# Optimization experiments

Measured on AMD Instinct MI355X. Metric: run time of the kernel, lower is better.

Reference implementation:

```python
import jax, jax.numpy as jnp
import numpy as np

B, S, H, K = 64, 512, 768, 21  # batch, seq_len, bert hidden, num_labels


def setup_inputs() -> dict:
    key = jax.random.key(0)
    ks = jax.random.split(key, 8)
    hidden = jax.random.normal(ks[0], (B, S, H), jnp.float32)  # post-BERT states
    W = jax.random.normal(ks[1], (H, K), jnp.float32) * 0.02    # classifier weight
    b = jnp.zeros((K,), jnp.float32)                            # classifier bias
    start_transitions = jax.random.uniform(ks[2], (K,), jnp.float32, -0.1, 0.1)
    transitions = jax.random.uniform(ks[3], (K, K), jnp.float32, -0.1, 0.1)
    end_transitions = jax.random.uniform(ks[4], (K,), jnp.float32, -0.1, 0.1)
    labels = jax.random.randint(ks[5], (B, S), 0, K)
    # torchcrf requires mask[:, 0] == 1; use variable-length prefix masks
    lengths = jax.random.randint(ks[6], (B,), S // 2, S + 1)
    attention_mask = jnp.arange(S)[None, :] < lengths[:, None]  # [B,S] bool
    return dict(hidden=hidden, W=W, b=b,
                start_transitions=start_transitions,
                transitions=transitions,
                end_transitions=end_transitions,
                labels=labels, attention_mask=attention_mask)


def _crf_nll(logits, labels, mask, start_t, trans, end_t):
    """torchcrf CRF forward (reduction='sum' log-likelihood), negated."""
    fmask = mask.astype(logits.dtype)  # [B,S]
    # ---- numerator: score of the gold path ----
    emit = jnp.take_along_axis(logits, labels[..., None], axis=2)[..., 0]  # [B,S]
    tr = trans[labels[:, :-1], labels[:, 1:]]                              # [B,S-1]
    num = start_t[labels[:, 0]] + emit[:, 0] \
        + jnp.sum((emit[:, 1:] + tr) * fmask[:, 1:], axis=1)
    lengths = mask.sum(axis=1)
    last_tags = jnp.take_along_axis(labels, (lengths - 1)[:, None], axis=1)[:, 0]
    num = num + end_t[last_tags]
    # ---- denominator: forward algorithm (logsumexp recurrence) ----
    alpha0 = start_t[None, :] + logits[:, 0]           # [B,K]
    ems = jnp.swapaxes(logits[:, 1:], 0, 1)            # [S-1,B,K]
    ms = jnp.swapaxes(mask[:, 1:], 0, 1)               # [S-1,B]

    def step(alpha, xs):
        em, m = xs
        nxt = jax.scipy.special.logsumexp(
            alpha[:, :, None] + trans[None, :, :] + em[:, None, :], axis=1)
        return jnp.where(m[:, None], nxt, alpha), None

    alpha, _ = jax.lax.scan(step, alpha0, (ems, ms))
    logZ = jax.scipy.special.logsumexp(alpha + end_t[None, :], axis=1)  # [B]
    return jnp.sum(logZ - num)  # negative log-likelihood (sum over batch)


def reference(hidden, W, b, start_transitions, transitions, end_transitions,
              labels, attention_mask):
    # dropout is identity in eval; the GRU in __init__ is unused in forward
    logits = hidden @ W + b  # [B,S,K]
    nll = _crf_nll(logits, labels, attention_mask,
                   start_transitions, transitions, end_transitions)
    # module returns (logits, -1 * log_likelihood) = (logits, nll)
    return (logits, nll)
```

## Files before the change

kernel.cpp:

```cpp
#include <hip/hip_runtime.h>

#define BSZ 64
#define SEQ 512
#define HID 768
#define NK  21

typedef short bf16x8 __attribute__((ext_vector_type(8)));
typedef float f32x4  __attribute__((ext_vector_type(4)));

__device__ __forceinline__ unsigned f2bf1(float x) {
    unsigned u = __float_as_uint(x);
    return (u + 0x7fffu + ((u >> 16) & 1u)) >> 16;
}
__device__ __forceinline__ unsigned f2bf_pk(float lo, float hi) {
    return f2bf1(lo) | (f2bf1(hi) << 16);
}

__global__ __launch_bounds__(256) void wconv_kernel(
    const float* __restrict__ W, unsigned short* __restrict__ WT)
{
    const int idx = blockIdx.x * 256 + threadIdx.x;
    const int n = idx / HID;
    const int k = idx - n * HID;
    unsigned short v = 0;
    if (n < NK) v = (unsigned short)f2bf1(W[(size_t)k * NK + n]);
    WT[idx] = v;
}

__global__ __launch_bounds__(256) void gemm_bias_kernel(
    const float* __restrict__ hidden, const unsigned short* __restrict__ WT,
    const float* __restrict__ bias, float* __restrict__ out)
{
    const int tid  = threadIdx.x;
    const int lane = tid & 63;
    const int wv   = tid >> 6;
    const int n    = lane & 15;
    const int quad = lane >> 4;

    const int arow = blockIdx.x * 64 + wv * 16 + n;
    const float* ap = hidden + (size_t)arow * HID + quad * 8;
    const bf16x8* bp0 = (const bf16x8*)(WT + (size_t)n * HID + quad * 8);
    const bf16x8* bp1 = (const bf16x8*)(WT + (size_t)(16 + n) * HID + quad * 8);

    f32x4 acc0 = {0.f, 0.f, 0.f, 0.f};
    f32x4 acc1 = {0.f, 0.f, 0.f, 0.f};

    float4 c0a = *(const float4*)(ap + 0);
    float4 c0b = *(const float4*)(ap + 4);

    #pragma unroll
    for (int c = 0; c < HID / 32; ++c) {
        float4 c1a, c1b;
        if (c + 1 < HID / 32) {
            c1a = *(const float4*)(ap + (c + 1) * 32);
            c1b = *(const float4*)(ap + (c + 1) * 32 + 4);
        }
        union { bf16x8 v; unsigned u[4]; } af;
        af.u[0] = f2bf_pk(c0a.x, c0a.y);
        af.u[1] = f2bf_pk(c0a.z, c0a.w);
        af.u[2] = f2bf_pk(c0b.x, c0b.y);
        af.u[3] = f2bf_pk(c0b.z, c0b.w);

        const bf16x8 b0 = bp0[c * 4];
        const bf16x8 b1 = bp1[c * 4];

        acc0 = __builtin_amdgcn_mfma_f32_16x16x32_bf16(af.v, b0, acc0, 0, 0, 0);
        acc1 = __builtin_amdgcn_mfma_f32_16x16x32_bf16(af.v, b1, acc1, 0, 0, 0);
        c0a = c1a; c0b = c1b;
    }

    const float b0v = bias[n];
    const float b1v = (n < NK - 16) ? bias[16 + n] : 0.f;
    const int rbase = blockIdx.x * 64 + wv * 16 + quad * 4;
    #pragma unroll
    for (int r = 0; r < 4; ++r) {
        float* op = out + (size_t)(rbase + r) * NK;
        op[n] = acc0[r] + b0v;
        if (n < NK - 16) op[16 + n] = acc1[r] + b1v;
    }
}

__global__ __launch_bounds__(128) void crf_kernel(
    const float* __restrict__ logits,
    const float* __restrict__ start_t,
    const float* __restrict__ trans,
    const float* __restrict__ end_t,
    const int* __restrict__ labels,
    const int* __restrict__ mask,
    float* __restrict__ per_batch)
{
    __shared__ __align__(16) float Xl[SEQ * NK];
    __shared__ float C[SEQ];
    __shared__ float comb[24];

    const int b    = blockIdx.x;
    const int tid  = threadIdx.x;
    const int lane = tid & 63;
    const int wid  = tid >> 6;

    {
        const float4* g4 = (const float4*)(logits + (size_t)b * SEQ * NK);
        float4* l4 = (float4*)Xl;
        for (int idx = tid; idx < SEQ * NK / 4; idx += 128) l4[idx] = g4[idx];
    }

    const int* lab = labels + b * SEQ;
    const int* msk = mask   + b * SEQ;

    int cnt = 0;
    for (int t = lane; t < SEQ; t += 64) cnt += (msk[t] != 0);
    #pragma unroll
    for (int off = 32; off > 0; off >>= 1) cnt += __shfl_xor(cnt, off, 64);
    const int L = cnt;
    const int m = L >> 1;

    __syncthreads();

    {
        float numacc = 0.f;
        for (int t = tid; t < L; t += 128) {
            if (t == 0) numacc += start_t[lab[0]] + Xl[lab[0]];
            else        numacc += Xl[t * NK + lab[t]] + trans[lab[t - 1] * NK + lab[t]];
        }
        if (tid == 0) numacc += end_t[lab[L - 1]];
        #pragma unroll
        for (int off = 32; off > 0; off >>= 1) numacc += __shfl_xor(numacc, off, 64);
        if (lane == 0) comb[22 + wid] = numacc;
    }

    for (int t = tid; t < SEQ; t += 128) C[t] = Xl[t * NK];
    __syncthreads();

    for (int idx = tid; idx < SEQ * NK; idx += 128) {
        const int t = idx / NK;
        Xl[idx] = __expf(Xl[idx] - C[t]);
    }
    __syncthreads();

    const int jj = (lane < NK) ? lane : NK - 1;

#define BP(v, k) __uint_as_float(__builtin_amdgcn_ds_bpermute(4 * (k), __float_as_uint(v)))
#define MATVEC(vv, EE, outv) do {                                          \
    float s0 = BP(vv, 0) * EE[0];                                          \
    float s1 = BP(vv, 1) * EE[1];                                          \
    float s2 = BP(vv, 2) * EE[2];                                          \
    s0 = fmaf(BP(vv,  3), EE[ 3], s0); s1 = fmaf(BP(vv,  4), EE[ 4], s1);  \
    s2 = fmaf(BP(vv,  5), EE[ 5], s2); s0 = fmaf(BP(vv,  6), EE[ 6], s0);  \
    s1 = fmaf(BP(vv,  7), EE[ 7], s1); s2 = fmaf(BP(vv,  8), EE[ 8], s2);  \
    s0 = fmaf(BP(vv,  9), EE[ 9], s0); s1 = fmaf(BP(vv, 10), EE[10], s1);  \
    s2 = fmaf(BP(vv, 11), EE[11], s2); s0 = fmaf(BP(vv, 12), EE[12], s0);  \
    s1 = fmaf(BP(vv, 13), EE[13], s1); s2 = fmaf(BP(vv, 14), EE[14], s2);  \
    s0 = fmaf(BP(vv, 15), EE[15], s0); s1 = fmaf(BP(vv, 16), EE[16], s1);  \
    s2 = fmaf(BP(vv, 17), EE[17], s2); s0 = fmaf(BP(vv, 18), EE[18], s0);  \
    s1 = fmaf(BP(vv, 19), EE[19], s1); s2 = fmaf(BP(vv, 20), EE[20], s2);  \
    outv = (s0 + s1) + s2;                                                 \
} while (0)
#define RENORM() do {                                                      \
    const float mm = __uint_as_float(                                      \
        __builtin_amdgcn_readfirstlane(__float_as_uint(a)));               \
    a *= __builtin_amdgcn_rcpf(mm);                                        \
    Orenorm += __logf(mm);                                                 \
} while (0)

    float a;
    float Orenorm = 0.f;
    float csum = 0.f;

    if (wid == 0) {
        float Ecol[NK];
        #pragma unroll
        for (int k = 0; k < NK; ++k) Ecol[k] = __expf(trans[k * NK + jj]);

        a = __expf(start_t[jj]) * Xl[jj];
        for (int t = lane; t <= m; t += 64) csum += C[t];

#define FSTEP(xr) do { float nv; MATVEC(a, Ecol, nv); a = nv * (xr); } while (0)
        int t0 = 1;
        for (; t0 + 7 <= m; t0 += 8) {
            const float* xb = Xl + t0 * NK + jj;
            const float x0 = xb[0];      const float x1 = xb[NK];
            const float x2 = xb[2 * NK]; const float x3 = xb[3 * NK];
            const float x4 = xb[4 * NK]; const float x5 = xb[5 * NK];
            const float x6 = xb[6 * NK]; const float x7 = xb[7 * NK];
            FSTEP(x0); FSTEP(x1); FSTEP(x2); FSTEP(x3);
            FSTEP(x4); FSTEP(x5); FSTEP(x6); FSTEP(x7);
            RENORM();
        }
        for (; t0 <= m; ++t0) { const float x = Xl[t0 * NK + jj]; FSTEP(x); }
#undef FSTEP
    } else {
        float Erow[NK];
        #pragma unroll
        for (int k = 0; k < NK; ++k) Erow[k] = __expf(trans[jj * NK + k]);

        a = __expf(end_t[jj]);
        for (int t = m + 1 + lane; t < L; t += 64) csum += C[t];

#define BSTEP(xr) do { const float u = a * (xr); float nv; MATVEC(u, Erow, nv); a = nv; } while (0)
        int t0 = L - 1;
        for (; t0 - 7 >= m + 1; t0 -= 8) {
            const float* xb = Xl + t0 * NK + jj;
            const float x0 = xb[0];       const float x1 = xb[-NK];
            const float x2 = xb[-2 * NK]; const float x3 = xb[-3 * NK];
            const float x4 = xb[-4 * NK]; const float x5 = xb[-5 * NK];
            const float x6 = xb[-6 * NK]; const float x7 = xb[-7 * NK];
            BSTEP(x0); BSTEP(x1); BSTEP(x2); BSTEP(x3);
            BSTEP(x4); BSTEP(x5); BSTEP(x6); BSTEP(x7);
            RENORM();
        }
        for (; t0 >= m + 1; --t0) { const float x = Xl[t0 * NK + jj]; BSTEP(x); }
#undef BSTEP
    }
#undef BP
#undef MATVEC
#undef RENORM

    #pragma unroll
    for (int off = 32; off > 0; off >>= 1) csum += __shfl_xor(csum, off, 64);

    if (wid == 1) {
        if (lane < NK) comb[lane] = a;
        if (lane == 0) comb[21] = csum + Orenorm;
    }
    __syncthreads();

    if (wid == 0) {
        float val = (lane < NK) ? a * comb[lane] : 0.f;
        #pragma unroll
        for (int off = 32; off > 0; off >>= 1) val += __shfl_xor(val, off, 64);
        if (lane == 0) {
            const float OF  = csum + Orenorm;
            const float num = comb[22] + comb[23];
            per_batch[b] = OF + comb[21] + __logf(val) - num;
        }
    }
}

__global__ __launch_bounds__(64) void reduce_kernel(
    const float* __restrict__ pb, float* __restrict__ out)
{
    float v = pb[threadIdx.x];
    #pragma unroll
    for (int off = 32; off > 0; off >>= 1) v += __shfl_xor(v, off, 64);
    if (threadIdx.x == 0) out[BSZ * SEQ * NK] = v;
}

extern "C" void kernel_launch(void* const* d_in, const int* in_sizes, int n_in,
                              void* d_out, int out_size, void* d_ws, size_t ws_size,
                              hipStream_t stream)
{
    const float* hidden  = (const float*)d_in[0];
    const float* W       = (const float*)d_in[1];
    const float* bias    = (const float*)d_in[2];
    const float* start_t = (const float*)d_in[3];
    const float* trans   = (const float*)d_in[4];
    const float* end_t   = (const float*)d_in[5];
    const int*   labels  = (const int*)d_in[6];
    const int*   mask    = (const int*)d_in[7];
    float* out = (float*)d_out;

    float*          pb = (float*)d_ws;
    unsigned short* WT = (unsigned short*)((char*)d_ws + 256);

    wconv_kernel<<<(32 * HID) / 256, 256, 0, stream>>>(W, WT);
    gemm_bias_kernel<<<(BSZ * SEQ) / 64, 256, 0, stream>>>(hidden, WT, bias, out);
    crf_kernel<<<BSZ, 128, 0, stream>>>(out, start_t, trans, end_t, labels, mask, pb);
    reduce_kernel<<<1, 64, 0, stream>>>(pb, out);
}
```

Baseline: 208.3 us.

## Parallelize CRF forward recurrence via segment transfer-matrix prepass and short scan

Replaces the serial 512-step per-batch CRF recurrence with a prepass kernel that, for each of 64 segments of 8 timesteps per batch, multiplies out the 21x21 transfer matrices in parallel, normalizing and logging the scale factors. A scan kernel then chains only 32 segment matrices forward and 32 backward per batch, using readlane instead of bpermute. This aims to shorten the latency-bound sequential chain and raise occupancy. In exchange it adds a large workspace write and readback of segment matrices, more total flops, and relies on per-segment renormalization for numerical range.

```diff
diff --git a/kernel.cpp b/kernel.cpp
--- a/kernel.cpp
+++ b/kernel.cpp
@@ -4,6 +4,8 @@
 #define SEQ 512
 #define HID 768
 #define NK  21
+#define NSEG 64
+#define SEGLEN 8
 
 typedef short bf16x8 __attribute__((ext_vector_type(8)));
 typedef float f32x4  __attribute__((ext_vector_type(4)));
@@ -80,47 +82,135 @@
     }
 }
 
-__global__ __launch_bounds__(128) void crf_kernel(
+__global__ __launch_bounds__(64) void prepass_kernel(
+    const float* __restrict__ logits, const float* __restrict__ trans,
+    const int* __restrict__ mask,
+    float* __restrict__ Nrow, float* __restrict__ Ncol,
+    float* __restrict__ rlog)
+{
+    const int bs   = blockIdx.x;
+    const int b    = bs >> 6;
+    const int s    = bs & 63;
+    const int lane = threadIdx.x;
+    int g = lane / 21; if (g > 2) g = 2;
+    int i = lane - g * 21; if (i > 20) i = 20;
+    const int j0 = 7 * g;
+
+    const int* msk = mask + b * SEQ;
+    int cnt = 0;
+    #pragma unroll
+    for (int t = 0; t < SEQ / 64; ++t) cnt += (msk[lane + 64 * t] != 0);
+    #pragma unroll
+    for (int off = 32; off > 0; off >>= 1) cnt += __shfl_xor(cnt, off, 64);
+    const int L = cnt;
+
+    float E[21][7];
+    #pragma unroll
+    for (int k = 0; k < 21; ++k)
+        #pragma unroll
+        for (int jl = 0; jl < 7; ++jl)
+            E[k][jl] = __expf(trans[k * NK + j0 + jl]);
+
+    const float* lg = logits + (size_t)b * SEQ * NK;
+
+    float P[7];
+    float rl = 0.f;
+    const int t0 = s * SEGLEN + 1;
+
+    if (t0 < L) {
+        const float C = lg[t0 * NK];
+        #pragma unroll
+        for (int jl = 0; jl < 7; ++jl)
+            P[jl] = E[i][jl] * __expf(lg[t0 * NK + j0 + jl] - C);
+    } else {
+        #pragma unroll
+        for (int jl = 0; jl < 7; ++jl) P[jl] = (i == j0 + jl) ? 1.f : 0.f;
+    }
+
+#define BPF(v, idx) __uint_as_float(__builtin_amdgcn_ds_bpermute((idx) * 4, __float_as_uint(v)))
+
+    #pragma unroll
+    for (int u = 1; u < SEGLEN; ++u) {
+        const int t = t0 + u;
+        if (t < L) {
+            float row[21];
+            #pragma unroll
+            for (int k = 0; k < 21; ++k)
+                row[k] = BPF(P[k % 7], (k / 7) * 21 + i);
+
+            const float C = lg[t * NK];
+            float X[7];
+            #pragma unroll
+            for (int jl = 0; jl < 7; ++jl)
+                X[jl] = __expf(lg[t * NK + j0 + jl] - C);
+
+            #pragma unroll
+            for (int jl = 0; jl < 7; ++jl) {
+                float s0 = row[0] * E[0][jl];
+                float s1 = row[1] * E[1][jl];
+                float s2 = row[2] * E[2][jl];
+                #pragma unroll
+                for (int k = 3; k < 21; k += 3) {
+                    s0 = fmaf(row[k    ], E[k    ][jl], s0);
+                    s1 = fmaf(row[k + 1], E[k + 1][jl], s1);
+                    s2 = fmaf(row[k + 2], E[k + 2][jl], s2);
+                }
+                P[jl] = ((s0 + s1) + s2) * X[jl];
+            }
+            const float m = BPF(P[0], 0);
+            const float r = __builtin_amdgcn_rcpf(m);
+            #pragma unroll
+            for (int jl = 0; jl < 7; ++jl) P[jl] *= r;
+            rl += __logf(m);
+        }
+    }
+#undef BPF
+
+    if (lane < 63) {
+        float* nr = Nrow + (size_t)bs * 441 + i * 21 + j0;
+        #pragma unroll
+        for (int jl = 0; jl < 7; ++jl) nr[jl] = P[jl];
+        float* nc = Ncol + (size_t)bs * 441 + i;
+        #pragma unroll
+        for (int jl = 0; jl < 7; ++jl) nc[(j0 + jl) * 21] = P[jl];
+    }
+    if (lane == 0) rlog[bs] = rl;
+}
+
+__global__ __launch_bounds__(128) void scan_kernel(
     const float* __restrict__ logits,
     const float* __restrict__ start_t,
     const float* __restrict__ trans,
     const float* __restrict__ end_t,
     const int* __restrict__ labels,
     const int* __restrict__ mask,
+    const float* __restrict__ Nrow, const float* __restrict__ Ncol,
+    const float* __restrict__ rlog,
     float* __restrict__ per_batch)
 {
-    __shared__ __align__(16) float Xl[SEQ * NK];
-    __shared__ float C[SEQ];
-    __shared__ float comb[24];
+    __shared__ float comb[26];
 
     const int b    = blockIdx.x;
     const int tid  = threadIdx.x;
     const int lane = tid & 63;
     const int wid  = tid >> 6;
 
-    {
-        const float4* g4 = (const float4*)(logits + (size_t)b * SEQ * NK);
-        float4* l4 = (float4*)Xl;
-        for (int idx = tid; idx < SEQ * NK / 4; idx += 128) l4[idx] = g4[idx];
-    }
-
+    const float* lg = logits + (size_t)b * SEQ * NK;
     const int* lab = labels + b * SEQ;
     const int* msk = mask   + b * SEQ;
 
     int cnt = 0;
-    for (int t = lane; t < SEQ; t += 64) cnt += (msk[t] != 0);
+    #pragma unroll
+    for (int t = 0; t < SEQ / 64; ++t) cnt += (msk[lane + 64 * t] != 0);
     #pragma unroll
     for (int off = 32; off > 0; off >>= 1) cnt += __shfl_xor(cnt, off, 64);
     const int L = cnt;
-    const int m = L >> 1;
-
-    __syncthreads();
 
     {
         float numacc = 0.f;
         for (int t = tid; t < L; t += 128) {
-            if (t == 0) numacc += start_t[lab[0]] + Xl[lab[0]];
-            else        numacc += Xl[t * NK + lab[t]] + trans[lab[t - 1] * NK + lab[t]];
+            if (t == 0) numacc += start_t[lab[0]] + lg[lab[0]];
+            else        numacc += lg[t * NK + lab[t]] + trans[lab[t - 1] * NK + lab[t]];
         }
         if (tid == 0) numacc += end_t[lab[L - 1]];
         #pragma unroll
@@ -128,99 +218,91 @@
         if (lane == 0) comb[22 + wid] = numacc;
     }
 
-    for (int t = tid; t < SEQ; t += 128) C[t] = Xl[t * NK];
-    __syncthreads();
-
-    for (int idx = tid; idx < SEQ * NK; idx += 128) {
-        const int t = idx / NK;
-        Xl[idx] = __expf(Xl[idx] - C[t]);
-    }
-    __syncthreads();
+    float rls = (lane < 32) ? rlog[b * NSEG + wid * 32 + lane] : 0.f;
+    #pragma unroll
+    for (int off = 32; off > 0; off >>= 1) rls += __shfl_xor(rls, off, 64);
 
     const int jj = (lane < NK) ? lane : NK - 1;
 
-#define BP(v, k) __uint_as_float(__builtin_amdgcn_ds_bpermute(4 * (k), __float_as_uint(v)))
-#define MATVEC(vv, EE, outv) do {                                          \
-    float s0 = BP(vv, 0) * EE[0];                                          \
-    float s1 = BP(vv, 1) * EE[1];                                          \
-    float s2 = BP(vv, 2) * EE[2];                                          \
-    s0 = fmaf(BP(vv,  3), EE[ 3], s0); s1 = fmaf(BP(vv,  4), EE[ 4], s1);  \
-    s2 = fmaf(BP(vv,  5), EE[ 5], s2); s0 = fmaf(BP(vv,  6), EE[ 6], s0);  \
-    s1 = fmaf(BP(vv,  7), EE[ 7], s1); s2 = fmaf(BP(vv,  8), EE[ 8], s2);  \
-    s0 = fmaf(BP(vv,  9), EE[ 9], s0); s1 = fmaf(BP(vv, 10), EE[10], s1);  \
-    s2 = fmaf(BP(vv, 11), EE[11], s2); s0 = fmaf(BP(vv, 12), EE[12], s0);  \
-    s1 = fmaf(BP(vv, 13), EE[13], s1); s2 = fmaf(BP(vv, 14), EE[14], s2);  \
-    s0 = fmaf(BP(vv, 15), EE[15], s0); s1 = fmaf(BP(vv, 16), EE[16], s1);  \
-    s2 = fmaf(BP(vv, 17), EE[17], s2); s0 = fmaf(BP(vv, 18), EE[18], s0);  \
-    s1 = fmaf(BP(vv, 19), EE[19], s1); s2 = fmaf(BP(vv, 20), EE[20], s2);  \
-    outv = (s0 + s1) + s2;                                                 \
-} while (0)
-#define RENORM() do {                                                      \
-    const float mm = __uint_as_float(                                      \
-        __builtin_amdgcn_readfirstlane(__float_as_uint(a)));               \
-    a *= __builtin_amdgcn_rcpf(mm);                                        \
-    Orenorm += __logf(mm);                                                 \
-} while (0)
-
-    float a;
-    float Orenorm = 0.f;
-    float csum = 0.f;
+#define RL(v, k) __uint_as_float(__builtin_amdgcn_readlane(__float_as_uint(v), k))
+
+    float a, csum = 0.f, Orenorm = 0.f;
+    float ncur[21], nnx[21];
 
     if (wid == 0) {
-        float Ecol[NK];
-        #pragma unroll
-        for (int k = 0; k < NK; ++k) Ecol[k] = __expf(trans[k * NK + jj]);
-
-        a = __expf(start_t[jj]) * Xl[jj];
-        for (int t = lane; t <= m; t += 64) csum += C[t];
-
-#define FSTEP(xr) do { float nv; MATVEC(a, Ecol, nv); a = nv * (xr); } while (0)
-        int t0 = 1;
-        for (; t0 + 7 <= m; t0 += 8) {
-            const float* xb = Xl + t0 * NK + jj;
-            const float x0 = xb[0];      const float x1 = xb[NK];
-            const float x2 = xb[2 * NK]; const float x3 = xb[3 * NK];
-            const float x4 = xb[4 * NK]; const float x5 = xb[5 * NK];
-            const float x6 = xb[6 * NK]; const float x7 = xb[7 * NK];
-            FSTEP(x0); FSTEP(x1); FSTEP(x2); FSTEP(x3);
-            FSTEP(x4); FSTEP(x5); FSTEP(x6); FSTEP(x7);
-            RENORM();
-        }
-        for (; t0 <= m; ++t0) { const float x = Xl[t0 * NK + jj]; FSTEP(x); }
-#undef FSTEP
+        const int hi = (L < 256) ? L : 256;
+        for (int t = lane; t < hi; t += 64) csum += lg[t * NK];
+        a = __expf(start_t[jj]) * __expf(lg[jj] - lg[0]);
+
+        const float* base = Ncol + (size_t)b * NSEG * 441 + jj * 21;
+        #pragma unroll
+        for (int k = 0; k < 21; ++k) ncur[k] = base[k];
+        for (int s = 0; s < 32; ++s) {
+            if (s < 31) {
+                const float* p = base + (size_t)(s + 1) * 441;
+                #pragma unroll
+                for (int k = 0; k < 21; ++k) nnx[k] = p[k];
+            }
+            float s0 = RL(a, 0) * ncur[0];
+            float s1 = RL(a, 1) * ncur[1];
+            float s2 = RL(a, 2) * ncur[2];
+            #pragma unroll
+            for (int k = 3; k < 21; k += 3) {
+                s0 = fmaf(RL(a, k    ), ncur[k    ], s0);
+                s1 = fmaf(RL(a, k + 1), ncur[k + 1], s1);
+                s2 = fmaf(RL(a, k + 2), ncur[k + 2], s2);
+            }
+            a = (s0 + s1) + s2;
+            const float m = __uint_as_float(
+                __builtin_amdgcn_readfirstlane(__float_as_uint(a)));
+            a *= __builtin_amdgcn_rcpf(m);
+            Orenorm += __logf(m);
+            if (s < 31) {
+                #pragma unroll
+                for (int k = 0; k < 21; ++k) ncur[k] = nnx[k];
+            }
+        }
     } else {
-        float Erow[NK];
-        #pragma unroll
-        for (int k = 0; k < NK; ++k) Erow[k] = __expf(trans[jj * NK + k]);
-
+        for (int t = 256 + lane; t < L; t += 64) csum += lg[t * NK];
         a = __expf(end_t[jj]);
-        for (int t = m + 1 + lane; t < L; t += 64) csum += C[t];
-
-#define BSTEP(xr) do { const float u = a * (xr); float nv; MATVEC(u, Erow, nv); a = nv; } while (0)
-        int t0 = L - 1;
-        for (; t0 - 7 >= m + 1; t0 -= 8) {
-            const float* xb = Xl + t0 * NK + jj;
-            const float x0 = xb[0];       const float x1 = xb[-NK];
-            const float x2 = xb[-2 * NK]; const float x3 = xb[-3 * NK];
-            const float x4 = xb[-4 * NK]; const float x5 = xb[-5 * NK];
-            const float x6 = xb[-6 * NK]; const float x7 = xb[-7 * NK];
-            BSTEP(x0); BSTEP(x1); BSTEP(x2); BSTEP(x3);
-            BSTEP(x4); BSTEP(x5); BSTEP(x6); BSTEP(x7);
-            RENORM();
-        }
-        for (; t0 >= m + 1; --t0) { const float x = Xl[t0 * NK + jj]; BSTEP(x); }
-#undef BSTEP
-    }
-#undef BP
-#undef MATVEC
-#undef RENORM
+
+        const float* base = Nrow + (size_t)b * NSEG * 441 + jj * 21;
+        #pragma unroll
+        for (int k = 0; k < 21; ++k) ncur[k] = base[(size_t)63 * 441 + k];
+        for (int s = 63; s >= 32; --s) {
+            if (s > 32) {
+                const float* p = base + (size_t)(s - 1) * 441;
+                #pragma unroll
+                for (int k = 0; k < 21; ++k) nnx[k] = p[k];
+            }
+            float s0 = RL(a, 0) * ncur[0];
+            float s1 = RL(a, 1) * ncur[1];
+            float s2 = RL(a, 2) * ncur[2];
+            #pragma unroll
+            for (int k = 3; k < 21; k += 3) {
+                s0 = fmaf(RL(a, k    ), ncur[k    ], s0);
+                s1 = fmaf(RL(a, k + 1), ncur[k + 1], s1);
+                s2 = fmaf(RL(a, k + 2), ncur[k + 2], s2);
+            }
+            a = (s0 + s1) + s2;
+            const float m = __uint_as_float(
+                __builtin_amdgcn_readfirstlane(__float_as_uint(a)));
+            a *= __builtin_amdgcn_rcpf(m);
+            Orenorm += __logf(m);
+            if (s > 32) {
+                #pragma unroll
+                for (int k = 0; k < 21; ++k) ncur[k] = nnx[k];
+            }
+        }
+    }
+#undef RL
 
     #pragma unroll
     for (int off = 32; off > 0; off >>= 1) csum += __shfl_xor(csum, off, 64);
 
     if (wid == 1) {
         if (lane < NK) comb[lane] = a;
-        if (lane == 0) comb[21] = csum + Orenorm;
+        if (lane == 0) comb[21] = csum + Orenorm + rls;
     }
     __syncthreads();
 
@@ -229,7 +311,7 @@
         #pragma unroll
         for (int off = 32; off > 0; off >>= 1) val += __shfl_xor(val, off, 64);
         if (lane == 0) {
-            const float OF  = csum + Orenorm;
+            const float OF  = csum + Orenorm + rls;
             const float num = comb[22] + comb[23];
             per_batch[b] = OF + comb[21] + __logf(val) - num;
         }
@@ -259,11 +341,17 @@
     const int*   mask    = (const int*)d_in[7];
     float* out = (float*)d_out;
 
-    float*          pb = (float*)d_ws;
-    unsigned short* WT = (unsigned short*)((char*)d_ws + 256);
+    unsigned short* WT = (unsigned short*)d_ws;
+    float* f    = (float*)((char*)d_ws + 65536);
+    float* pb   = f;
+    float* rlog = f + 64;
+    float* Nrow = f + 8192;
+    float* Ncol = Nrow + BSZ * NSEG * 441;
 
     wconv_kernel<<<(32 * HID) / 256, 256, 0, stream>>>(W, WT);
     gemm_bias_kernel<<<(BSZ * SEQ) / 64, 256, 0, stream>>>(hidden, WT, bias, out);
-    crf_kernel<<<BSZ, 128, 0, stream>>>(out, start_t, trans, end_t, labels, mask, pb);
+    prepass_kernel<<<BSZ * NSEG, 64, 0, stream>>>(out, trans, mask, Nrow, Ncol, rlog);
+    scan_kernel<<<BSZ, 128, 0, stream>>>(out, start_t, trans, end_t, labels, mask,
+                                         Nrow, Ncol, rlog, pb);
     reduce_kernel<<<1, 64, 0, stream>>>(pb, out);
 }
```

Result: slower. 245.2 us (+17.7%).
